# Optimization experiments

Hardware: AMD Instinct MI355X
Metric: run time of the kernel (lower is better)

Reference implementation:

```python
import jax, jax.numpy as jnp
import numpy as np

N = 100_000      # nodes
E = 1_600_000    # edges (avg degree 16)
IN = 512         # in_feats
HID = 4          # hidden_feats (forced equal to num_heads=4 by the mean(h,2) in forward)
H1 = 4           # heads in layer 1
OUT = 128        # out_feats
NEG_SLOPE = 0.2  # DGL GATConv leaky_relu default


def setup_inputs() -> dict:
    key = jax.random.key(0)
    ks = jax.random.split(key, 12)
    nfeats = jax.random.normal(ks[0], (N, IN), jnp.float32)
    efeats = jax.random.normal(ks[1], (E, 8), jnp.float32)  # unused by the module
    src = jax.random.randint(ks[2], (E,), 0, N, dtype=jnp.int32)
    dst = jax.random.randint(ks[3], (E,), 0, N, dtype=jnp.int32)
    # layer 1 params (in=IN, heads=H1, per-head out=HID)
    fc1_w = jax.random.normal(ks[4], (IN, H1 * HID), jnp.float32) / np.sqrt(IN)
    attn_l1 = jax.random.normal(ks[5], (H1, HID), jnp.float32) / np.sqrt(HID)
    attn_r1 = jax.random.normal(ks[6], (H1, HID), jnp.float32) / np.sqrt(HID)
    bias1 = jnp.zeros((H1 * HID,), jnp.float32)
    # layer 2 params (in=H1=4 after mean over feature dim, heads=1, out=OUT)
    fc2_w = jax.random.normal(ks[7], (HID, 1 * OUT), jnp.float32) / np.sqrt(HID)
    attn_l2 = jax.random.normal(ks[8], (1, OUT), jnp.float32) / np.sqrt(OUT)
    attn_r2 = jax.random.normal(ks[9], (1, OUT), jnp.float32) / np.sqrt(OUT)
    bias2 = jnp.zeros((OUT,), jnp.float32)
    return {"nfeats": nfeats, "efeats": efeats, "src": src, "dst": dst,
            "fc1_w": fc1_w, "attn_l1": attn_l1, "attn_r1": attn_r1, "bias1": bias1,
            "fc2_w": fc2_w, "attn_l2": attn_l2, "attn_r2": attn_r2, "bias2": bias2}


def gat_layer(x, src, dst, fc_w, attn_l, attn_r, bias, heads, d_out):
    # projection: (N, in) -> (N, H, D)
    h = (x @ fc_w).reshape(-1, heads, d_out)
    el = jnp.einsum('nhd,hd->nh', h, attn_l)   # (N, H)
    er = jnp.einsum('nhd,hd->nh', h, attn_r)
    e = jax.nn.leaky_relu(el[src] + er[dst], NEG_SLOPE)  # (E, H)
    # segment softmax over incoming edges of each dst node
    m = jax.lax.stop_gradient(jax.ops.segment_max(e, dst, num_segments=N))
    ex = jnp.exp(e - m[dst])
    denom = jax.ops.segment_sum(ex, dst, num_segments=N)
    alpha = ex / denom[dst]                    # (E, H)
    msg = alpha[:, :, None] * h[src]           # (E, H, D)
    rst = jax.ops.segment_sum(msg, dst, num_segments=N)  # (N, H, D)
    return rst + bias.reshape(1, heads, d_out)


def reference(nfeats, efeats, src, dst, fc1_w, attn_l1, attn_r1, bias1,
              fc2_w, attn_l2, attn_r2, bias2):
    h = gat_layer(nfeats, src, dst, fc1_w, attn_l1, attn_r1, bias1, H1, HID)  # (N,4,4)
    h = jnp.mean(h, axis=2)        # faithful to th.mean(h, 2): mean over per-head feat dim -> (N,4)
    h = jax.nn.relu(h)
    h = gat_layer(h, src, dst, fc2_w, attn_l2, attn_r2, bias2, 1, OUT)        # (N,1,OUT)
    return h.reshape(N, OUT)       # flatten(1)
```

## Files before the change

### kernel.cpp

```cpp
#include <hip/hip_runtime.h>
#include <math.h>

#define IN_F 512
#define OUTF 128
#define NEG_SLOPE 0.2f

typedef __attribute__((ext_vector_type(8))) short bf16x8;
typedef __attribute__((ext_vector_type(4))) float f32x4;
typedef __attribute__((ext_vector_type(4))) unsigned u32x4;
typedef const __attribute__((address_space(1))) void gvoid;
typedef __attribute__((address_space(3))) void lvoid;

#define P1T 256
#define NKS 16
#define BPSH 8192
#define TW 64
#define TILE_B (16 * TW * 4)
#define RING 3

#define NPB 128
#define NBMAX 784
#define EPB 8192
#define SRCMASK 0x1FFFF
#define CAP 2944

#define SMEM_A (4 * RING * TILE_B)

__device__ __forceinline__ unsigned pkbf(float a, float b) {
  unsigned ua = __float_as_uint(a); ua += 0x7FFF + ((ua >> 16) & 1);
  unsigned ub = __float_as_uint(b); ub += 0x7FFF + ((ub >> 16) & 1);
  return (ua >> 16) | (ub & 0xFFFF0000u);
}

#define VMCNT8() do { asm volatile("s_waitcnt vmcnt(8)" ::: "memory"); \
                      __builtin_amdgcn_sched_barrier(0); } while (0)
#define VMCNT4() do { asm volatile("s_waitcnt vmcnt(4)" ::: "memory"); \
                      __builtin_amdgcn_sched_barrier(0); } while (0)
#define VMCNT0() do { asm volatile("s_waitcnt vmcnt(0)" ::: "memory"); \
                      __builtin_amdgcn_sched_barrier(0); } while (0)

__device__ __forceinline__ void issue_tile(const float* __restrict__ x, int wrow,
                                           int kbase, char* lbase, int lane) {
#pragma unroll
  for (int i = 0; i < 4; ++i) {
    int f = lane + i * 64;
    int r = f >> 4, c16 = f & 15;
    int srcu = c16 ^ (r & 7);
    const float* g = x + (size_t)(wrow + r) * IN_F + kbase + srcu * 4;
    __builtin_amdgcn_global_load_lds((gvoid*)g, (lvoid*)(lbase + i * 1024), 16, 0, 0);
  }
}

__global__ void k_prep(const float* __restrict__ fc1, const float* __restrict__ al1,
                       const float* __restrict__ ar1, const float* __restrict__ fc2,
                       const float* __restrict__ al2, const float* __restrict__ ar2,
                       unsigned short* __restrict__ Bp,
                       float* __restrict__ w2al, float* __restrict__ w2ar,
                       int* __restrict__ bucketCursor) {
  __shared__ float wlds[IN_F * 12];
  int t = threadIdx.x;
  if (blockIdx.x == 0) {
    int k = t;
#pragma unroll
    for (int h = 0; h < 4; ++h) {
      float wl = 0.f, wr = 0.f, wb = 0.f;
#pragma unroll
      for (int j = 0; j < 4; ++j) {
        float wv = fc1[k * 16 + h * 4 + j];
        wl = fmaf(wv, al1[h * 4 + j], wl);
        wr = fmaf(wv, ar1[h * 4 + j], wr);
        wb += wv;
      }
      wlds[k * 12 + h] = wl;
      wlds[k * 12 + 4 + h] = wr;
      wlds[k * 12 + 8 + h] = 0.25f * wb;
    }
    __syncthreads();
    for (int item = t; item < NKS * 64; item += 512) {
      int s = item >> 6, l = item & 63;
      int col = l & 15;
      int kb = s * 32 + ((l >> 4) * 8);
      unsigned hi[4];
#pragma unroll
      for (int p = 0; p < 4; ++p) {
        float w0 = 0.f, w1 = 0.f;
        if (col < 12) {
          w0 = wlds[(kb + 2 * p) * 12 + col];
          w1 = wlds[(kb + 2 * p + 1) * 12 + col];
        }
        hi[p] = pkbf(w0, w1);
      }
      *(uint4*)&Bp[item * 8] = make_uint4(hi[0], hi[1], hi[2], hi[3]);
    }
  } else {
    if (t < 8) {
      int h = t >> 1;
      const float* a = (t & 1) ? ar2 : al2;
      float s = 0.f;
#pragma unroll 16
      for (int c = 0; c < OUTF; ++c) s += fc2[h * OUTF + c] * a[c];
      if (t & 1) w2ar[h] = s; else w2al[h] = s;
    }
    for (int i = t; i < NBMAX; i += 512) bucketCursor[i] = 0;
  }
}

__global__ __launch_bounds__(P1T) void k_A(
    const float* __restrict__ x, const unsigned short* __restrict__ Bp,
    float* __restrict__ pk1, float* __restrict__ er1, int n,
    const int* __restrict__ src, const int* __restrict__ dst,
    int* __restrict__ bucketCursor, unsigned* __restrict__ ep, int e,
    int binBlocks, int projBlocks)
{
  __shared__ __align__(16) char smem[SMEM_A];
  const int t = threadIdx.x;

  if ((int)blockIdx.x < binBlocks) {
    int* hist = (int*)smem;
    int* base = hist + NBMAX;
    int* lcur = base + NBMAX;
    const int bb = blockIdx.x;
    for (int i = t; i < NBMAX; i += P1T) hist[i] = 0;
    __syncthreads();
    int blockBase = bb * EPB;
#pragma unroll
    for (int i = 0; i < EPB / P1T; ++i) {
      int idx = blockBase + t + i * P1T;
      if (idx < e) atomicAdd(&hist[dst[idx] >> 7], 1);
    }
    __syncthreads();
    for (int i = t; i < NBMAX; i += P1T) {
      if (hist[i] > 0) base[i] = atomicAdd(&bucketCursor[i], hist[i]);
      lcur[i] = 0;
    }
    __syncthreads();
#pragma unroll
    for (int i = 0; i < EPB / P1T; ++i) {
      int idx = blockBase + t + i * P1T;
      if (idx < e) {
        int d = dst[idx];
        int b = d >> 7;
        int off = base[b] + atomicAdd(&lcur[b], 1);
        if (off < CAP)
          ep[(size_t)b * CAP + off] = (unsigned)src[idx] | ((unsigned)(d & (NPB - 1)) << 17);
      }
    }
  } else {
    const int pb = blockIdx.x - binBlocks;
    const int lane = t & 63;
    const int wv = t >> 6;
    char* ring = smem + (size_t)wv * (RING * TILE_B);

    bf16x8 Breg[NKS];
#pragma unroll
    for (int i = 0; i < NKS; ++i)
      Breg[i] = *(const bf16x8*)&Bp[(i * 64 + lane) * 8];

    const int R = lane & 15;
    const int g = lane >> 4;
    const int sw = R & 7;
    const int totalWaves = projBlocks * 4;
    const int rtMax = (n + 15) >> 4;

    for (int rt = pb * 4 + wv; rt < rtMax; rt += totalWaves) {
      const int wrow = rt * 16;
      f32x4 acc = {0.f, 0.f, 0.f, 0.f};

      issue_tile(x, wrow, 0, ring + 0 * TILE_B, lane);
      issue_tile(x, wrow, TW, ring + 1 * TILE_B, lane);

#pragma unroll
      for (int T = 0; T < 8; ++T) {
        if (T < 6) issue_tile(x, wrow, (T + 2) * TW, ring + ((T + 2) % 3) * TILE_B, lane);
        if (T < 6)      { VMCNT8(); }
        else if (T == 6){ VMCNT4(); }
        else            { VMCNT0(); }
        const char* lb = ring + (T % 3) * TILE_B;
#pragma unroll
        for (int ks = 0; ks < 2; ++ks) {
          int j16 = ks * 8 + g * 2;
          float4 a0 = *(const float4*)(lb + R * 256 + ((j16) ^ sw) * 16);
          float4 a1 = *(const float4*)(lb + R * 256 + ((j16 + 1) ^ sw) * 16);
          u32x4 au = {pkbf(a0.x, a0.y), pkbf(a0.z, a0.w),
                      pkbf(a1.x, a1.y), pkbf(a1.z, a1.w)};
          union { u32x4 u; bf16x8 v; } cvt; cvt.u = au;
          acc = __builtin_amdgcn_mfma_f32_16x16x32_bf16(cvt.v, Breg[T * 2 + ks],
                                                        acc, 0, 0, 0);
        }
      }

      int col = lane & 15;
      int rbase = wrow + (g * 4);
#pragma unroll
      for (int i = 0; i < 4; ++i) {
        int row = rbase + i;
        if (row < n) {
          float v = acc[i];
          if (col < 4)       pk1[(size_t)row * 8 + col] = v;
          else if (col < 8)  er1[(size_t)row * 4 + (col - 4)] = v;
          else if (col < 12) pk1[(size_t)row * 8 + 4 + (col - 8)] = v;
        }
      }
    }
  }
}

__global__ __launch_bounds__(256) void k_B(
    const unsigned* __restrict__ ep, const int* __restrict__ bucketCursor,
    unsigned* __restrict__ ep2, int* __restrict__ nodeBeg, int* __restrict__ nodeEnd,
    const float* __restrict__ pk1, const float* __restrict__ er1,
    const float* __restrict__ bias1,
    const float* __restrict__ w2al, const float* __restrict__ w2ar,
    float* __restrict__ pk2, float* __restrict__ er2, int n)
{
  __shared__ int cnt[NPB];
  __shared__ int scn[NPB];
  __shared__ int cur[NPB];
  __shared__ unsigned lbuf[CAP];
  int t = threadIdx.x;
  int b = blockIdx.x;
  int nodeBase = b * NPB;
  int m = bucketCursor[b];
  if (m > CAP) m = CAP;
  const unsigned* __restrict__ in = ep + (size_t)b * CAP;
  if (t < NPB) cnt[t] = 0;
  __syncthreads();
  for (int j = t; j < m; j += 256) atomicAdd(&cnt[in[j] >> 17], 1);
  __syncthreads();
  if (t < NPB) scn[t] = cnt[t];
  __syncthreads();
  for (int off = 1; off < NPB; off <<= 1) {
    int v = (t < NPB && t >= off) ? scn[t - off] : 0;
    __syncthreads();
    if (t < NPB) scn[t] += v;
    __syncthreads();
  }
  if (t < NPB) {
    int excl = scn[t] - cnt[t];
    int node = nodeBase + t;
    if (node < n) {
      nodeBeg[node] = b * CAP + excl;
      nodeEnd[node] = b * CAP + excl + cnt[t];
    }
    cur[t] = excl;
  }
  __syncthreads();
  for (int j = t; j < m; j += 256) {
    unsigned p = in[j];
    int pos = atomicAdd(&cur[p >> 17], 1);
    lbuf[pos] = p & SRCMASK;
  }
  __syncthreads();
  for (int i = t; i < m; i += 256) ep2[(size_t)b * CAP + i] = lbuf[i];

#pragma unroll
  for (int half = 0; half < 2; ++half) {
    int w = t + half * 256;
    int i = w >> 2, h = w & 3;
    int node = nodeBase + i;
    bool active = node < n;
    float v = 0.f;
    if (active) {
      int beg = scn[i] - cnt[i], end = scn[i];
      float ern = er1[(size_t)node * 4 + h];
      float den = 0.f, num = 0.f;
      for (int j = beg; j < end; ++j) {
        int s = (int)lbuf[j];
        float el = pk1[(size_t)s * 8 + h];
        float hb = pk1[(size_t)s * 8 + 4 + h];
        float eh = el + ern;
        eh = (eh > 0.f) ? eh : NEG_SLOPE * eh;
        float wg = __expf(eh);
        den += wg;
        num = fmaf(wg, hb, num);
      }
      float mb = 0.25f * (bias1[h*4] + bias1[h*4+1] + bias1[h*4+2] + bias1[h*4+3]);
      v = (end > beg) ? num / den : 0.f;
      v += mb;
      v = (v > 0.f) ? v : 0.f;
    }
    float pl = v * w2al[h];
    float pr = v * w2ar[h];
    pl += __shfl_xor(pl, 1); pl += __shfl_xor(pl, 2);
    pr += __shfl_xor(pr, 1); pr += __shfl_xor(pr, 2);
    if (active) {
      pk2[(size_t)node * 8 + h] = v;
      if (h == 0) { pk2[(size_t)node * 8 + 4] = pl; er2[node] = pr; }
    }
  }
}

__global__ __launch_bounds__(256) void k_bagg2(
    const unsigned* __restrict__ ep2, const int* __restrict__ nodeBeg,
    const int* __restrict__ nodeEnd,
    const float* __restrict__ pk2, const float* __restrict__ er2,
    const float* __restrict__ w2, const float* __restrict__ bias2,
    float* __restrict__ out, int n)
{
  __shared__ float gacc[256 * 4];
  __shared__ float w2s[4 * OUTF];
  __shared__ float b2s[OUTF];
  int t = threadIdx.x;
  int nodeBase = blockIdx.x * 256;
  int nn = nodeBase + t;
  for (int i = t; i < 4 * OUTF; i += 256) w2s[i] = w2[i];
  if (t < OUTF) b2s[t] = bias2[t];
  float g0 = 0.f, g1 = 0.f, g2 = 0.f, g3 = 0.f;
  if (nn < n) {
    int beg = nodeBeg[nn], end = nodeEnd[nn];
    float ern = er2[nn];
    float den = 0.f;
    for (int j = beg; j < end; ++j) {
      int s = (int)ep2[j];
      const float* __restrict__ ps = &pk2[(size_t)s * 8];
      float4 hv = *(const float4*)ps;
      float e = ps[4] + ern;
      e = (e > 0.f) ? e : NEG_SLOPE * e;
      float w = __expf(e);
      den += w;
      g0 = fmaf(w, hv.x, g0); g1 = fmaf(w, hv.y, g1);
      g2 = fmaf(w, hv.z, g2); g3 = fmaf(w, hv.w, g3);
    }
    float inv = (end > beg) ? 1.0f / den : 0.f;
    g0 *= inv; g1 *= inv; g2 *= inv; g3 *= inv;
  }
  gacc[t * 4 + 0] = g0; gacc[t * 4 + 1] = g1;
  gacc[t * 4 + 2] = g2; gacc[t * 4 + 3] = g3;
  __syncthreads();
  for (int idx = t; idx < 256 * (OUTF / 2); idx += 256) {
    int i = idx >> 6;
    int node = nodeBase + i;
    if (node >= n) continue;
    int c = (idx & 63) * 2;
    float gx = gacc[i*4], gy = gacc[i*4+1], gz = gacc[i*4+2], gw = gacc[i*4+3];
    float2 o;
    o.x = gx*w2s[c]   + gy*w2s[OUTF+c]   + gz*w2s[2*OUTF+c]   + gw*w2s[3*OUTF+c]   + b2s[c];
    o.y = gx*w2s[c+1] + gy*w2s[OUTF+c+1] + gz*w2s[2*OUTF+c+1] + gw*w2s[3*OUTF+c+1] + b2s[c+1];
    *(float2*)&out[(size_t)node * OUTF + c] = o;
  }
}

extern "C" void kernel_launch(void* const* d_in, const int* in_sizes, int n_in,
                              void* d_out, int out_size, void* d_ws, size_t ws_size,
                              hipStream_t stream) {
  const float* nfeats = (const float*)d_in[0];
  const int*   srcp   = (const int*)d_in[2];
  const int*   dstp   = (const int*)d_in[3];
  const float* fc1    = (const float*)d_in[4];
  const float* al1    = (const float*)d_in[5];
  const float* ar1    = (const float*)d_in[6];
  const float* bias1  = (const float*)d_in[7];
  const float* fc2    = (const float*)d_in[8];
  const float* al2    = (const float*)d_in[9];
  const float* ar2    = (const float*)d_in[10];
  const float* bias2  = (const float*)d_in[11];

  const int N = in_sizes[0] / IN_F;
  const int E = in_sizes[2];
  const int NB = (N + NPB - 1) / NPB;

  float* ws   = (float*)d_ws;
  float* pk1  = ws;
  float* er1  = pk1 + (size_t)8 * N;
  float* pk2  = er1 + (size_t)4 * N;
  float* er2  = pk2 + (size_t)8 * N;
  float* w2al = er2 + N;
  float* w2ar = w2al + 4;
  unsigned short* Bp = (unsigned short*)(w2ar + 4);
  int* bucketCursor = (int*)(Bp + BPSH);
  int* nodeBeg      = bucketCursor + NBMAX;
  int* nodeEnd      = nodeBeg + N;
  unsigned* ep      = (unsigned*)(nodeEnd + N);
  unsigned* ep2     = ep + (size_t)NB * CAP;

  const int binBlocks = (E + EPB - 1) / EPB;
  const int projBlocks = 572;

  k_prep<<<2, 512, 0, stream>>>(fc1, al1, ar1, fc2, al2, ar2,
                                Bp, w2al, w2ar, bucketCursor);
  k_A<<<binBlocks + projBlocks, P1T, 0, stream>>>(nfeats, Bp, pk1, er1, N,
                                                  srcp, dstp, bucketCursor, ep, E,
                                                  binBlocks, projBlocks);
  k_B<<<NB, 256, 0, stream>>>(ep, bucketCursor, ep2, nodeBeg, nodeEnd,
                              pk1, er1, bias1, w2al, w2ar, pk2, er2, N);
  k_bagg2<<<(N + 255) / 256, 256, 0, stream>>>(ep2, nodeBeg, nodeEnd, pk2, er2,
                                               fc2, bias2, (float*)d_out, N);
}
```

Baseline: 133.1 us.

## Replace LDS staging with register-prefetched direct global loads in projection

New measurement: 137.9 us. 3.6% more time.

```diff
diff --git a/kernel.cpp b/kernel.cpp
--- a/kernel.cpp
+++ b/kernel.cpp
@@ -8,15 +8,11 @@
 typedef __attribute__((ext_vector_type(8))) short bf16x8;
 typedef __attribute__((ext_vector_type(4))) float f32x4;
 typedef __attribute__((ext_vector_type(4))) unsigned u32x4;
-typedef const __attribute__((address_space(1))) void gvoid;
-typedef __attribute__((address_space(3))) void lvoid;
 
 #define P1T 256
 #define NKS 16
+#define PFD 4
 #define BPSH 8192
-#define TW 64
-#define TILE_B (16 * TW * 4)
-#define RING 3
 
 #define NPB 128
 #define NBMAX 784
@@ -24,31 +20,10 @@
 #define SRCMASK 0x1FFFF
 #define CAP 2944
 
-#define SMEM_A (4 * RING * TILE_B)
-
 __device__ __forceinline__ unsigned pkbf(float a, float b) {
   unsigned ua = __float_as_uint(a); ua += 0x7FFF + ((ua >> 16) & 1);
   unsigned ub = __float_as_uint(b); ub += 0x7FFF + ((ub >> 16) & 1);
   return (ua >> 16) | (ub & 0xFFFF0000u);
-}
-
-#define VMCNT8() do { asm volatile("s_waitcnt vmcnt(8)" ::: "memory"); \
-                      __builtin_amdgcn_sched_barrier(0); } while (0)
-#define VMCNT4() do { asm volatile("s_waitcnt vmcnt(4)" ::: "memory"); \
-                      __builtin_amdgcn_sched_barrier(0); } while (0)
-#define VMCNT0() do { asm volatile("s_waitcnt vmcnt(0)" ::: "memory"); \
-                      __builtin_amdgcn_sched_barrier(0); } while (0)
-
-__device__ __forceinline__ void issue_tile(const float* __restrict__ x, int wrow,
-                                           int kbase, char* lbase, int lane) {
-#pragma unroll
-  for (int i = 0; i < 4; ++i) {
-    int f = lane + i * 64;
-    int r = f >> 4, c16 = f & 15;
-    int srcu = c16 ^ (r & 7);
-    const float* g = x + (size_t)(wrow + r) * IN_F + kbase + srcu * 4;
-    __builtin_amdgcn_global_load_lds((gvoid*)g, (lvoid*)(lbase + i * 1024), 16, 0, 0);
-  }
 }
 
 __global__ void k_prep(const float* __restrict__ fc1, const float* __restrict__ al1,
@@ -79,15 +54,16 @@
     for (int item = t; item < NKS * 64; item += 512) {
       int s = item >> 6, l = item & 63;
       int col = l & 15;
-      int kb = s * 32 + ((l >> 4) * 8);
+      int g = l >> 4;
+      int kb = s * 32;
       unsigned hi[4];
 #pragma unroll
       for (int p = 0; p < 4; ++p) {
-        float w0 = 0.f, w1 = 0.f;
-        if (col < 12) {
-          w0 = wlds[(kb + 2 * p) * 12 + col];
-          w1 = wlds[(kb + 2 * p + 1) * 12 + col];
-        }
+        int e0 = 2 * p, e1 = 2 * p + 1;
+        int k0 = kb + ((e0 < 4) ? (g * 4 + e0) : (16 + g * 4 + e0 - 4));
+        int k1 = kb + ((e1 < 4) ? (g * 4 + e1) : (16 + g * 4 + e1 - 4));
+        float w0 = (col < 12) ? wlds[k0 * 12 + col] : 0.f;
+        float w1 = (col < 12) ? wlds[k1 * 12 + col] : 0.f;
         hi[p] = pkbf(w0, w1);
       }
       *(uint4*)&Bp[item * 8] = make_uint4(hi[0], hi[1], hi[2], hi[3]);
@@ -112,13 +88,12 @@
     int* __restrict__ bucketCursor, unsigned* __restrict__ ep, int e,
     int binBlocks, int projBlocks)
 {
-  __shared__ __align__(16) char smem[SMEM_A];
+  __shared__ int hist[NBMAX];
+  __shared__ int base[NBMAX];
+  __shared__ int lcur[NBMAX];
   const int t = threadIdx.x;
 
   if ((int)blockIdx.x < binBlocks) {
-    int* hist = (int*)smem;
-    int* base = hist + NBMAX;
-    int* lcur = base + NBMAX;
     const int bb = blockIdx.x;
     for (int i = t; i < NBMAX; i += P1T) hist[i] = 0;
     __syncthreads();
@@ -149,57 +124,61 @@
     const int pb = blockIdx.x - binBlocks;
     const int lane = t & 63;
     const int wv = t >> 6;
-    char* ring = smem + (size_t)wv * (RING * TILE_B);
+    const int R = lane & 15;
+    const int g = lane >> 4;
 
     bf16x8 Breg[NKS];
 #pragma unroll
     for (int i = 0; i < NKS; ++i)
       Breg[i] = *(const bf16x8*)&Bp[(i * 64 + lane) * 8];
 
-    const int R = lane & 15;
-    const int g = lane >> 4;
-    const int sw = R & 7;
     const int totalWaves = projBlocks * 4;
+    const long tileStride = (long)totalWaves * 16 * IN_F;
     const int rtMax = (n + 15) >> 4;
-
-    for (int rt = pb * 4 + wv; rt < rtMax; rt += totalWaves) {
-      const int wrow = rt * 16;
-      f32x4 acc = {0.f, 0.f, 0.f, 0.f};
-
-      issue_tile(x, wrow, 0, ring + 0 * TILE_B, lane);
-      issue_tile(x, wrow, TW, ring + 1 * TILE_B, lane);
-
-#pragma unroll
-      for (int T = 0; T < 8; ++T) {
-        if (T < 6) issue_tile(x, wrow, (T + 2) * TW, ring + ((T + 2) % 3) * TILE_B, lane);
-        if (T < 6)      { VMCNT8(); }
-        else if (T == 6){ VMCNT4(); }
-        else            { VMCNT0(); }
-        const char* lb = ring + (T % 3) * TILE_B;
-#pragma unroll
-        for (int ks = 0; ks < 2; ++ks) {
-          int j16 = ks * 8 + g * 2;
-          float4 a0 = *(const float4*)(lb + R * 256 + ((j16) ^ sw) * 16);
-          float4 a1 = *(const float4*)(lb + R * 256 + ((j16 + 1) ^ sw) * 16);
+    const int rt0 = pb * 4 + wv;
+    if (rt0 < rtMax) {
+      const float* xr = x + (size_t)(rt0 * 16 + R) * IN_F + g * 4;
+
+      float4 q[PFD][2];
+#pragma unroll
+      for (int p = 0; p < PFD; ++p) {
+        q[p][0] = *(const float4*)&xr[p * 32];
+        q[p][1] = *(const float4*)&xr[p * 32 + 16];
+      }
+
+      for (int rt = rt0; rt < rtMax; rt += totalWaves) {
+        const bool hasNext = (rt + totalWaves) < rtMax;
+        const float* xrN = xr + tileStride;
+        f32x4 acc = {0.f, 0.f, 0.f, 0.f};
+
+#pragma unroll
+        for (int ks = 0; ks < NKS; ++ks) {
+          const int slot = ks & (PFD - 1);
+          float4 a0 = q[slot][0], a1 = q[slot][1];
+          if (ks + PFD < NKS) {
+            q[slot][0] = *(const float4*)&xr[(ks + PFD) * 32];
+            q[slot][1] = *(const float4*)&xr[(ks + PFD) * 32 + 16];
+          } else if (hasNext) {
+            q[slot][0] = *(const float4*)&xrN[(ks + PFD - NKS) * 32];
+            q[slot][1] = *(const float4*)&xrN[(ks + PFD - NKS) * 32 + 16];
+          }
           u32x4 au = {pkbf(a0.x, a0.y), pkbf(a0.z, a0.w),
                       pkbf(a1.x, a1.y), pkbf(a1.z, a1.w)};
           union { u32x4 u; bf16x8 v; } cvt; cvt.u = au;
-          acc = __builtin_amdgcn_mfma_f32_16x16x32_bf16(cvt.v, Breg[T * 2 + ks],
-                                                        acc, 0, 0, 0);
+          acc = __builtin_amdgcn_mfma_f32_16x16x32_bf16(cvt.v, Breg[ks], acc, 0, 0, 0);
         }
-      }
-
-      int col = lane & 15;
-      int rbase = wrow + (g * 4);
-#pragma unroll
-      for (int i = 0; i < 4; ++i) {
-        int row = rbase + i;
-        if (row < n) {
+
+        int col = lane & 15;
+        int rbase = rt * 16 + (g * 4);
+#pragma unroll
+        for (int i = 0; i < 4; ++i) {
+          int row = rbase + i;
           float v = acc[i];
           if (col < 4)       pk1[(size_t)row * 8 + col] = v;
           else if (col < 8)  er1[(size_t)row * 4 + (col - 4)] = v;
           else if (col < 12) pk1[(size_t)row * 8 + 4 + (col - 8)] = v;
         }
+        xr = xrN;
       }
     }
   }
@@ -374,7 +353,7 @@
   unsigned* ep2     = ep + (size_t)NB * CAP;
 
   const int binBlocks = (E + EPB - 1) / EPB;
-  const int projBlocks = 572;
+  const int projBlocks = 828;
 
   k_prep<<<2, 512, 0, stream>>>(fc1, al1, ar1, fc2, al2, ar2,
                                 Bp, w2al, w2ar, bucketCursor);
```
